# Optimization experiments

Hardware: AMD Instinct MI355X
Metric: run time of the kernel (lower is better)

## Reference

```python
import jax, jax.numpy as jnp
import numpy as np

B, D, L, C, N = 4096, 256, 4, 2048, 100000
MARGIN = 0.2
EPS = 1e-12  # F.normalize eps


def _l2norm(x):
    return x / jnp.clip(jnp.linalg.norm(x, axis=-1, keepdims=True), EPS)


def setup_inputs() -> dict:
    key = jax.random.key(0)
    k1, k2, k3, k4 = jax.random.split(key, 4)
    anchors = jax.random.normal(k1, (B, D), dtype=jnp.float32)
    centroids = jax.random.normal(k2, (L, C, D), dtype=jnp.float32)
    # unique cluster labels 0..C-1 within each eps level
    centroid_labels = jnp.tile(jnp.arange(C, dtype=jnp.int32), (L, 1))
    # DBSCAN labels in {-1, 0, ..., C-1}; -1 = noise (no positive at that eps)
    labels_per_eps = jax.random.randint(k3, (L, N), 0, C + 1, dtype=jnp.int32) - 1
    local_indices = jax.random.randint(k4, (B,), 0, N, dtype=jnp.int32)
    return {
        "anchors": anchors,
        "centroids": centroids,
        "centroid_labels": centroid_labels,
        "labels_per_eps": labels_per_eps,
        "local_indices": local_indices,
    }


def reference(anchors, centroids, centroid_labels, labels_per_eps, local_indices):
    an = _l2norm(anchors)                                   # [B, D]
    cent = _l2norm(jax.lax.stop_gradient(centroids))        # centroids detached in original
    flat_c = cent.reshape(L * C, D)                         # [M, D]
    flat_eps = jnp.repeat(jnp.arange(L, dtype=jnp.int32), C)  # [M] eps id of each centroid
    flat_lab = centroid_labels.reshape(-1)                  # [M]

    anchor_labels = labels_per_eps[:, local_indices].T      # [B, L]
    lab_at = anchor_labels[:, flat_eps]                     # [B, M] anchor's label at centroid's eps
    pos = (lab_at == flat_lab[None, :]) & (lab_at != -1)    # [B, M] positive-centroid mask

    sim = an @ flat_c.T                                     # [B, M] cosine sims
    sim_ap = jnp.min(jnp.where(pos, sim, 2.0), axis=1)      # hardest positive (min sim)
    sim_an = jnp.max(jnp.where(pos, -2.0, sim), axis=1)     # hardest negative (max sim)

    has_pos = jnp.any(pos, axis=1)
    has_neg = jnp.any(~pos, axis=1)
    valid = has_pos & has_neg

    per = jnp.maximum(sim_an - sim_ap + MARGIN, 0.0)        # [B]
    cnt = jnp.sum(valid.astype(jnp.float32))
    loss = jnp.sum(jnp.where(valid, per, 0.0)) / jnp.maximum(cnt, 1.0)
    return loss
```

## Files before the change

### kernel.cpp

```cpp
#include <hip/hip_runtime.h>
#include <hip/hip_bf16.h>

#define BB 4096
#define DD 256
#define LL 4
#define CC 2048
#define NN 100000

typedef unsigned int uint32;

using f32x16 = __attribute__((ext_vector_type(16))) float;
using bf16x8 = __attribute__((ext_vector_type(8))) __bf16;

#define GLD16(g, l)                                                        \
    __builtin_amdgcn_global_load_lds(                                      \
        (const __attribute__((address_space(1))) unsigned int*)(g),        \
        (__attribute__((address_space(3))) unsigned int*)(l), 16, 0, 0)

__device__ __forceinline__ uint32 f2ord(float f) {
    uint32 u = __float_as_uint(f);
    return (u & 0x80000000u) ? ~u : (u | 0x80000000u);
}
__device__ __forceinline__ float ord2f(uint32 u) {
    u = (u & 0x80000000u) ? (u & 0x7FFFFFFFu) : ~u;
    return __uint_as_float(u);
}
__device__ __forceinline__ unsigned short bf16bits(float f) {
    __hip_bfloat16 h = __float2bfloat16(f);
    unsigned short b;
    __builtin_memcpy(&b, &h, 2);
    return b;
}


__global__ __launch_bounds__(256) void prep_all(const float* __restrict__ anchors,
                                                const float* __restrict__ centroids,
                                                const int* __restrict__ lpe,
                                                const int* __restrict__ li,
                                                unsigned short* __restrict__ Ah,
                                                unsigned short* __restrict__ Al,
                                                unsigned short* __restrict__ Ch,
                                                unsigned short* __restrict__ Cl,
                                                int* __restrict__ pos_col) {
    const int bid = blockIdx.x;
    if (bid >= 3072) {
        int t = (bid - 3072) * 256 + threadIdx.x;
        int l = t >> 12, b = t & 4095;
        pos_col[l * BB + b] = lpe[l * NN + li[b]];
        return;
    }
    const bool is_a = (bid < 1024);
    const float* src = is_a ? anchors : centroids;
    unsigned short* hi = is_a ? Ah : Ch;
    unsigned short* lo = is_a ? Al : Cl;
    const int rb = is_a ? bid : (bid - 1024);
    int row = rb * 4 + (threadIdx.x >> 6);
    int lane = threadIdx.x & 63;
    float4 v = *reinterpret_cast<const float4*>(src + (size_t)row * DD + lane * 4);
    float ss = v.x * v.x + v.y * v.y + v.z * v.z + v.w * v.w;
    #pragma unroll
    for (int m = 1; m < 64; m <<= 1) ss += __shfl_xor(ss, m);
    float inv = 1.0f / fmaxf(sqrtf(ss), 1e-12f);
    float y0 = v.x * inv, y1 = v.y * inv, y2 = v.z * inv, y3 = v.w * inv;
    ushort4 h, l;
    h.x = bf16bits(y0); l.x = bf16bits(y0 - __bfloat162float(__float2bfloat16(y0)));
    h.y = bf16bits(y1); l.y = bf16bits(y1 - __bfloat162float(__float2bfloat16(y1)));
    h.z = bf16bits(y2); l.z = bf16bits(y2 - __bfloat162float(__float2bfloat16(y2)));
    h.w = bf16bits(y3); l.w = bf16bits(y3 - __bfloat162float(__float2bfloat16(y3)));
    *reinterpret_cast<ushort4*>(hi + (size_t)row * DD + lane * 4) = h;
    *reinterpret_cast<ushort4*>(lo + (size_t)row * DD + lane * 4) = l;
}

__global__ __launch_bounds__(256, 4) void mfma_main(
    const unsigned short* __restrict__ Ah, const unsigned short* __restrict__ Al,
    const unsigned short* __restrict__ Bh, const unsigned short* __restrict__ Bl,
    const int* __restrict__ clab, const int* __restrict__ pos_col,
    float* __restrict__ pn, float* __restrict__ pp) {
    __shared__ __align__(16) char smem[32768];

    const int tid = threadIdx.x;
    const int lane = tid & 63;
    const int w = tid >> 6;
    const int wr = w >> 1, wc = w & 1;

    const int bid = blockIdx.x;
    const int xcd = bid & 7, inner = bid >> 3;
    const int bx = (xcd & 1) * 16 + (inner & 15);
    const int by = (xcd >> 1) * 16 + (inner >> 4);
    const int mb = bx * 128, nb = by * 128;
    const int lev = nb >> 11;

    const unsigned short* arr = (w == 0) ? Ah : (w == 1) ? Al : (w == 2) ? Bh : Bl;
    const int pbase = (w < 2) ? mb : nb;
    const int sblk = (lane & 3) ^ ((lane >> 3) & 3);
    const unsigned short* gbase =
        arr + (size_t)(pbase + (lane >> 2)) * DD + sblk * 8;
    char* lbase = smem + w * 8192;

    f32x16 zero = {};
    f32x16 acc[2][2];
    #pragma unroll
    for (int i = 0; i < 2; ++i)
        #pragma unroll
        for (int j = 0; j < 2; ++j) acc[i][j] = zero;

    const int hw = lane >> 5;
    const int l31 = lane & 31;
    const int bswz = (lane >> 1) & 3;

    for (int t = 0; t < 8; ++t) {
        __syncthreads();
        #pragma unroll
        for (int s = 0; s < 8; ++s)
            GLD16(gbase + s * 16 * DD + t * 32, lbase + s * 1024);
        __syncthreads();

        #pragma unroll
        for (int tt = 0; tt < 2; ++tt) {
            const int phys = (((tt * 2 + hw) ^ bswz) << 4);
            bf16x8 fah[2], fal[2], fbh[2], fbl[2];
            #pragma unroll
            for (int i = 0; i < 2; ++i) {
                const int ra = (wr * 64 + i * 32 + l31) * 64 + phys;
                fah[i] = *reinterpret_cast<const bf16x8*>(smem + ra);
                fal[i] = *reinterpret_cast<const bf16x8*>(smem + 8192 + ra);
                const int rb2 = (wc * 64 + i * 32 + l31) * 64 + phys;
                fbh[i] = *reinterpret_cast<const bf16x8*>(smem + 16384 + rb2);
                fbl[i] = *reinterpret_cast<const bf16x8*>(smem + 24576 + rb2);
            }
            #pragma unroll
            for (int i = 0; i < 2; ++i)
                #pragma unroll
                for (int j = 0; j < 2; ++j) {
                    acc[i][j] = __builtin_amdgcn_mfma_f32_32x32x16_bf16(
                        fah[i], fbh[j], acc[i][j], 0, 0, 0);
                    acc[i][j] = __builtin_amdgcn_mfma_f32_32x32x16_bf16(
                        fah[i], fbl[j], acc[i][j], 0, 0, 0);
                    acc[i][j] = __builtin_amdgcn_mfma_f32_32x32x16_bf16(
                        fal[i], fbh[j], acc[i][j], 0, 0, 0);
                }
        }
    }

    __syncthreads();
    float* Ln = reinterpret_cast<float*>(smem);
    float* Lp = reinterpret_cast<float*>(smem + 1024);

    const int cl0 = clab[nb + wc * 64 + l31];
    const int cl1 = clab[nb + wc * 64 + 32 + l31];
    #pragma unroll
    for (int i = 0; i < 2; ++i) {
        const int rl0 = wr * 64 + i * 32;
        #pragma unroll
        for (int q = 0; q < 4; ++q) {
            const int4 pc4 = *reinterpret_cast<const int4*>(
                &pos_col[lev * BB + mb + rl0 + 8 * q + 4 * hw]);
            #pragma unroll
            for (int e = 0; e < 4; ++e) {
                const int reg = 4 * q + e;
                const int pcv = (e == 0) ? pc4.x : (e == 1) ? pc4.y : (e == 2) ? pc4.z : pc4.w;
                const float s0 = acc[i][0][reg];
                const float s1 = acc[i][1][reg];
                const bool p0 = (pcv == cl0) && (pcv >= 0);
                const bool p1 = (pcv == cl1) && (pcv >= 0);
                float nm = fmaxf(p0 ? -2.f : s0, p1 ? -2.f : s1);
                float pm = fminf(p0 ? s0 : 2.f, p1 ? s1 : 2.f);
                #pragma unroll
                for (int m = 1; m < 32; m <<= 1) {
                    nm = fmaxf(nm, __shfl_xor(nm, m));
                    pm = fminf(pm, __shfl_xor(pm, m));
                }
                if (l31 == 0) {
                    const int idx = wc * 128 + rl0 + 8 * q + e + hw * 4;
                    Ln[idx] = nm;
                    Lp[idx] = pm;
                }
            }
        }
    }
    __syncthreads();
    if (tid < 128) {
        const float nm = fmaxf(Ln[tid], Ln[128 + tid]);
        const float pm = fminf(Lp[tid], Lp[128 + tid]);
        pn[(size_t)by * BB + mb + tid] = nm;
        pp[(size_t)by * BB + mb + tid] = pm;
    }
}

__global__ __launch_bounds__(256) void finalize1(const float* __restrict__ pn,
                                                 const float* __restrict__ pp,
                                                 float* __restrict__ partials) {
    const int tid = threadIdx.x;
    const int row = blockIdx.x * 256 + tid;
    float nm = -2.f, pm = 2.f;
    for (int y = 0; y < 64; ++y) {
        nm = fmaxf(nm, pn[(size_t)y * BB + row]);
        pm = fminf(pm, pp[(size_t)y * BB + row]);
    }
    float sum = 0.f, cnt = 0.f;
    if (pm < 1.5f) {
        sum = fmaxf(nm - pm + 0.2f, 0.f);
        cnt = 1.f;
    }
    #pragma unroll
    for (int m = 1; m < 64; m <<= 1) {
        sum += __shfl_xor(sum, m);
        cnt += __shfl_xor(cnt, m);
    }
    __shared__ float s4[4], c4[4];
    if ((tid & 63) == 0) { s4[tid >> 6] = sum; c4[tid >> 6] = cnt; }
    __syncthreads();
    if (tid == 0) {
        partials[blockIdx.x] = s4[0] + s4[1] + s4[2] + s4[3];
        partials[16 + blockIdx.x] = c4[0] + c4[1] + c4[2] + c4[3];
    }
}

__global__ void finalize2(const float* __restrict__ partials, float* __restrict__ out) {
    if (threadIdx.x == 0) {
        float S = 0.f, C = 0.f;
        for (int i = 0; i < 16; ++i) { S += partials[i]; C += partials[16 + i]; }
        out[0] = S / fmaxf(C, 1.f);
    }
}


__global__ __launch_bounds__(256) void inv_norms(const float* __restrict__ src,
                                                 float* __restrict__ dst, int nrows) {
    int row = blockIdx.x * 4 + (threadIdx.x >> 6);
    int lane = threadIdx.x & 63;
    if (row >= nrows) return;
    float4 v = *reinterpret_cast<const float4*>(src + (size_t)row * DD + lane * 4);
    float ss = v.x * v.x + v.y * v.y + v.z * v.z + v.w * v.w;
    #pragma unroll
    for (int m = 1; m < 64; m <<= 1) ss += __shfl_xor(ss, m);
    if (lane == 0) dst[row] = 1.0f / fmaxf(sqrtf(ss), 1e-12f);
}

__global__ __launch_bounds__(256) void prep_fb(const int* __restrict__ labels_per_eps,
                                               const int* __restrict__ local_indices,
                                               int* __restrict__ pos_col,
                                               uint32* __restrict__ ap_key,
                                               uint32* __restrict__ an_key) {
    int t = blockIdx.x * 256 + threadIdx.x;
    int b = t >> 2, l = t & 3;
    pos_col[t] = labels_per_eps[l * NN + local_indices[b]];
    if (t < BB) { ap_key[t] = f2ord(2.0f); an_key[t] = f2ord(-2.0f); }
}

__global__ __launch_bounds__(256, 4) void fp32_main(const float* __restrict__ A,
                                                    const float* __restrict__ Cm,
                                                    const float* __restrict__ inv_a,
                                                    const float* __restrict__ inv_c,
                                                    const int* __restrict__ clab,
                                                    const int* __restrict__ pos_col,
                                                    uint32* __restrict__ ap_key,
                                                    uint32* __restrict__ an_key) {
    __shared__ float4 As[64 * 17];
    __shared__ float4 Bs[16 * 64];
    const int tid = threadIdx.x;
    const int lane = tid & 63;
    const int wv = tid >> 6;
    const int mb = blockIdx.x * 64;
    const int colbase = blockIdx.y * 64;
    const int lev = colbase >> 11;
    const int kgS = tid & 15;
    const int rS = tid >> 4;
    float acc[16];
    #pragma unroll
    for (int r = 0; r < 16; ++r) acc[r] = 0.f;
    for (int kc = 0; kc < DD; kc += 64) {
        __syncthreads();
        #pragma unroll
        for (int i = 0; i < 4; ++i) {
            int r = rS + 16 * i;
            As[r * 17 + kgS] = *reinterpret_cast<const float4*>(
                A + (size_t)(mb + r) * DD + kc + kgS * 4);
            Bs[kgS * 64 + (r ^ (kgS & 7))] = *reinterpret_cast<const float4*>(
                Cm + (size_t)(colbase + r) * DD + kc + kgS * 4);
        }
        __syncthreads();
        #pragma unroll
        for (int kg = 0; kg < 16; ++kg) {
            float4 b = Bs[kg * 64 + (lane ^ (kg & 7))];
            #pragma unroll
            for (int r = 0; r < 16; ++r) {
                float4 a = As[(wv * 16 + r) * 17 + kg];
                acc[r] = fmaf(a.x, b.x, acc[r]);
                acc[r] = fmaf(a.y, b.y, acc[r]);
                acc[r] = fmaf(a.z, b.z, acc[r]);
                acc[r] = fmaf(a.w, b.w, acc[r]);
            }
        }
    }
    const float ic = inv_c[colbase + lane];
    const int cl = clab[colbase + lane];
    const int row0 = mb + wv * 16;
    #pragma unroll
    for (int r = 0; r < 16; ++r) {
        float s = acc[r] * inv_a[row0 + r] * ic;
        int pcr = pos_col[(row0 + r) * LL + lev];
        bool pos = (pcr == cl) && (pcr >= 0);
        float nm = pos ? -2.f : s;
        #pragma unroll
        for (int m = 1; m < 64; m <<= 1) nm = fmaxf(nm, __shfl_xor(nm, m));
        if (lane == 0) atomicMax(&an_key[row0 + r], f2ord(nm));
        if (pos) atomicMin(&ap_key[row0 + r], f2ord(s));
    }
}

__global__ __launch_bounds__(256) void fb_finalize(const uint32* __restrict__ ap_key,
                                                   const uint32* __restrict__ an_key,
                                                   float* __restrict__ out) {
    int tid = threadIdx.x;
    float sum = 0.f, cnt = 0.f;
    for (int b = tid; b < BB; b += 256) {
        float ap = ord2f(ap_key[b]);
        float an = ord2f(an_key[b]);
        if (ap < 1.5f) { sum += fmaxf(an - ap + 0.2f, 0.f); cnt += 1.f; }
    }
    #pragma unroll
    for (int m = 1; m < 64; m <<= 1) { sum += __shfl_xor(sum, m); cnt += __shfl_xor(cnt, m); }
    __shared__ float s4[4], c4[4];
    int w = tid >> 6;
    if ((tid & 63) == 0) { s4[w] = sum; c4[w] = cnt; }
    __syncthreads();
    if (tid == 0) {
        out[0] = (s4[0] + s4[1] + s4[2] + s4[3]) / fmaxf(c4[0] + c4[1] + c4[2] + c4[3], 1.f);
    }
}


extern "C" void kernel_launch(void* const* d_in, const int* in_sizes, int n_in,
                              void* d_out, int out_size, void* d_ws, size_t ws_size,
                              hipStream_t stream) {
    const float* anchors         = (const float*)d_in[0];
    const float* centroids       = (const float*)d_in[1];
    const int*   centroid_labels = (const int*)d_in[2];
    const int*   labels_per_eps  = (const int*)d_in[3];
    const int*   local_indices   = (const int*)d_in[4];
    float* out = (float*)d_out;

    const size_t MB = 1024 * 1024;
    if (ws_size >= 15 * MB) {
        char* ws = (char*)d_ws;
        unsigned short* Ah = (unsigned short*)(ws);
        unsigned short* Al = (unsigned short*)(ws + 2 * MB);
        unsigned short* Ch = (unsigned short*)(ws + 4 * MB);
        unsigned short* Cl = (unsigned short*)(ws + 8 * MB);
        int*   pos_col = (int*)(ws + 12 * MB);
        float* pn = (float*)(ws + 12 * MB + 256 * 1024);
        float* pp = (float*)(ws + 13 * MB + 256 * 1024);
        float* partials = (float*)(ws + 14 * MB + 256 * 1024);

        prep_all<<<3136, 256, 0, stream>>>(anchors, centroids, labels_per_eps,
                                           local_indices, Ah, Al, Ch, Cl, pos_col);
        mfma_main<<<2048, 256, 0, stream>>>(Ah, Al, Ch, Cl, centroid_labels,
                                            pos_col, pn, pp);
        finalize1<<<16, 256, 0, stream>>>(pn, pp, partials);
        finalize2<<<1, 64, 0, stream>>>(partials, out);
    } else {
        float*  inv_a  = (float*)d_ws;
        float*  inv_c  = inv_a + BB;
        int*    pos_col = (int*)(inv_c + LL * CC);
        uint32* ap_key = (uint32*)(pos_col + BB * LL);
        uint32* an_key = ap_key + BB;

        inv_norms<<<BB / 4, 256, 0, stream>>>(anchors, inv_a, BB);
        inv_norms<<<(LL * CC) / 4, 256, 0, stream>>>(centroids, inv_c, LL * CC);
        prep_fb<<<(BB * LL) / 256, 256, 0, stream>>>(labels_per_eps, local_indices,
                                                     pos_col, ap_key, an_key);
        fp32_main<<<dim3(BB / 64, 128), 256, 0, stream>>>(anchors, centroids, inv_a, inv_c,
                                                          centroid_labels, pos_col,
                                                          ap_key, an_key);
        fb_finalize<<<1, 256, 0, stream>>>(ap_key, an_key, out);
    }
}
```

Baseline: 148.6 us.

## Use single bf16 GEMM with per-group maxima and fp32 fixup of near-max candidates

Replaces the three-pass split-bf16 GEMM with a single bf16 pass that records the per-32-column-group hardest-negative maximum. A new fixup kernel recomputes in fp32 only those groups whose bf16 max lies within a 0.02 margin of the global max, and computes the single positive centroid similarity directly in fp32. The main loop also gains LDS double buffering so the next K slice loads while the current one feeds the MFMAs. The aim is to cut MFMA work roughly threefold and drop the lo-part buffers. The risk is that the fixed 0.02 margin must cover bf16 error, and the fixup assumes exactly one positive per level because labels are unique.

```diff
diff --git a/kernel.cpp b/kernel.cpp
--- a/kernel.cpp
+++ b/kernel.cpp
@@ -38,9 +38,9 @@
                                                 const int* __restrict__ lpe,
                                                 const int* __restrict__ li,
                                                 unsigned short* __restrict__ Ah,
-                                                unsigned short* __restrict__ Al,
                                                 unsigned short* __restrict__ Ch,
-                                                unsigned short* __restrict__ Cl,
+                                                float* __restrict__ inv_a,
+                                                float* __restrict__ inv_c,
                                                 int* __restrict__ pos_col) {
     const int bid = blockIdx.x;
     if (bid >= 3072) {
@@ -52,7 +52,6 @@
     const bool is_a = (bid < 1024);
     const float* src = is_a ? anchors : centroids;
     unsigned short* hi = is_a ? Ah : Ch;
-    unsigned short* lo = is_a ? Al : Cl;
     const int rb = is_a ? bid : (bid - 1024);
     int row = rb * 4 + (threadIdx.x >> 6);
     int lane = threadIdx.x & 63;
@@ -61,21 +60,19 @@
     #pragma unroll
     for (int m = 1; m < 64; m <<= 1) ss += __shfl_xor(ss, m);
     float inv = 1.0f / fmaxf(sqrtf(ss), 1e-12f);
-    float y0 = v.x * inv, y1 = v.y * inv, y2 = v.z * inv, y3 = v.w * inv;
-    ushort4 h, l;
-    h.x = bf16bits(y0); l.x = bf16bits(y0 - __bfloat162float(__float2bfloat16(y0)));
-    h.y = bf16bits(y1); l.y = bf16bits(y1 - __bfloat162float(__float2bfloat16(y1)));
-    h.z = bf16bits(y2); l.z = bf16bits(y2 - __bfloat162float(__float2bfloat16(y2)));
-    h.w = bf16bits(y3); l.w = bf16bits(y3 - __bfloat162float(__float2bfloat16(y3)));
+    ushort4 h;
+    h.x = bf16bits(v.x * inv);
+    h.y = bf16bits(v.y * inv);
+    h.z = bf16bits(v.z * inv);
+    h.w = bf16bits(v.w * inv);
     *reinterpret_cast<ushort4*>(hi + (size_t)row * DD + lane * 4) = h;
-    *reinterpret_cast<ushort4*>(lo + (size_t)row * DD + lane * 4) = l;
+    if (lane == 0) (is_a ? inv_a : inv_c)[row] = inv;
 }
 
 __global__ __launch_bounds__(256, 4) void mfma_main(
-    const unsigned short* __restrict__ Ah, const unsigned short* __restrict__ Al,
-    const unsigned short* __restrict__ Bh, const unsigned short* __restrict__ Bl,
+    const unsigned short* __restrict__ Ah, const unsigned short* __restrict__ Bh,
     const int* __restrict__ clab, const int* __restrict__ pos_col,
-    float* __restrict__ pn, float* __restrict__ pp) {
+    float* __restrict__ png) {
     __shared__ __align__(16) char smem[32768];
 
     const int tid = threadIdx.x;
@@ -90,12 +87,11 @@
     const int mb = bx * 128, nb = by * 128;
     const int lev = nb >> 11;
 
-    const unsigned short* arr = (w == 0) ? Ah : (w == 1) ? Al : (w == 2) ? Bh : Bl;
-    const int pbase = (w < 2) ? mb : nb;
+    const unsigned short* arr = (w < 2) ? Ah : Bh;
+    const int pbase = ((w < 2) ? mb : nb) + (w & 1) * 64;
     const int sblk = (lane & 3) ^ ((lane >> 3) & 3);
     const unsigned short* gbase =
         arr + (size_t)(pbase + (lane >> 2)) * DD + sblk * 8;
-    char* lbase = smem + w * 8192;
 
     f32x16 zero = {};
     f32x16 acc[2][2];
@@ -106,46 +102,45 @@
 
     const int hw = lane >> 5;
     const int l31 = lane & 31;
-    const int bswz = (lane >> 1) & 3;
-
+    const int bswz = (l31 >> 1) & 3;
+
+    #pragma unroll
+    for (int s = 0; s < 4; ++s)
+        GLD16(gbase + s * 16 * DD, smem + w * 4096 + s * 1024);
+    __syncthreads();
+
+    int buf = 0;
     for (int t = 0; t < 8; ++t) {
-        __syncthreads();
-        #pragma unroll
-        for (int s = 0; s < 8; ++s)
-            GLD16(gbase + s * 16 * DD + t * 32, lbase + s * 1024);
-        __syncthreads();
-
+        if (t < 7) {
+            char* lb = smem + (buf ^ 1) * 16384 + w * 4096;
+            #pragma unroll
+            for (int s = 0; s < 4; ++s)
+                GLD16(gbase + s * 16 * DD + (t + 1) * 32, lb + s * 1024);
+        }
+        const char* base = smem + buf * 16384;
         #pragma unroll
         for (int tt = 0; tt < 2; ++tt) {
             const int phys = (((tt * 2 + hw) ^ bswz) << 4);
-            bf16x8 fah[2], fal[2], fbh[2], fbl[2];
+            bf16x8 fa[2], fb[2];
             #pragma unroll
             for (int i = 0; i < 2; ++i) {
-                const int ra = (wr * 64 + i * 32 + l31) * 64 + phys;
-                fah[i] = *reinterpret_cast<const bf16x8*>(smem + ra);
-                fal[i] = *reinterpret_cast<const bf16x8*>(smem + 8192 + ra);
-                const int rb2 = (wc * 64 + i * 32 + l31) * 64 + phys;
-                fbh[i] = *reinterpret_cast<const bf16x8*>(smem + 16384 + rb2);
-                fbl[i] = *reinterpret_cast<const bf16x8*>(smem + 24576 + rb2);
+                fa[i] = *reinterpret_cast<const bf16x8*>(
+                    base + (wr * 64 + i * 32 + l31) * 64 + phys);
+                fb[i] = *reinterpret_cast<const bf16x8*>(
+                    base + 8192 + (wc * 64 + i * 32 + l31) * 64 + phys);
             }
             #pragma unroll
             for (int i = 0; i < 2; ++i)
                 #pragma unroll
-                for (int j = 0; j < 2; ++j) {
+                for (int j = 0; j < 2; ++j)
                     acc[i][j] = __builtin_amdgcn_mfma_f32_32x32x16_bf16(
-                        fah[i], fbh[j], acc[i][j], 0, 0, 0);
-                    acc[i][j] = __builtin_amdgcn_mfma_f32_32x32x16_bf16(
-                        fah[i], fbl[j], acc[i][j], 0, 0, 0);
-                    acc[i][j] = __builtin_amdgcn_mfma_f32_32x32x16_bf16(
-                        fal[i], fbh[j], acc[i][j], 0, 0, 0);
-                }
-        }
-    }
-
-    __syncthreads();
-    float* Ln = reinterpret_cast<float*>(smem);
-    float* Lp = reinterpret_cast<float*>(smem + 1024);
-
+                        fa[i], fb[j], acc[i][j], 0, 0, 0);
+        }
+        __syncthreads();
+        buf ^= 1;
+    }
+
+    float* Lg = reinterpret_cast<float*>(smem);
     const int cl0 = clab[nb + wc * 64 + l31];
     const int cl1 = clab[nb + wc * 64 + 32 + l31];
     #pragma unroll
@@ -158,69 +153,129 @@
             #pragma unroll
             for (int e = 0; e < 4; ++e) {
                 const int reg = 4 * q + e;
-                const int pcv = (e == 0) ? pc4.x : (e == 1) ? pc4.y : (e == 2) ? pc4.z : pc4.w;
-                const float s0 = acc[i][0][reg];
-                const float s1 = acc[i][1][reg];
-                const bool p0 = (pcv == cl0) && (pcv >= 0);
-                const bool p1 = (pcv == cl1) && (pcv >= 0);
-                float nm = fmaxf(p0 ? -2.f : s0, p1 ? -2.f : s1);
-                float pm = fminf(p0 ? s0 : 2.f, p1 ? s1 : 2.f);
+                const int pcv = (e == 0) ? pc4.x : (e == 1) ? pc4.y
+                              : (e == 2) ? pc4.z : pc4.w;
+                float n0 = ((pcv == cl0) && (pcv >= 0)) ? -2.f : acc[i][0][reg];
+                float n1 = ((pcv == cl1) && (pcv >= 0)) ? -2.f : acc[i][1][reg];
                 #pragma unroll
                 for (int m = 1; m < 32; m <<= 1) {
-                    nm = fmaxf(nm, __shfl_xor(nm, m));
-                    pm = fminf(pm, __shfl_xor(pm, m));
+                    n0 = fmaxf(n0, __shfl_xor(n0, m));
+                    n1 = fmaxf(n1, __shfl_xor(n1, m));
                 }
                 if (l31 == 0) {
-                    const int idx = wc * 128 + rl0 + 8 * q + e + hw * 4;
-                    Ln[idx] = nm;
-                    Lp[idx] = pm;
+                    const int rloc = rl0 + 8 * q + e + 4 * hw;
+                    Lg[(wc * 2 + 0) * 128 + rloc] = n0;
+                    Lg[(wc * 2 + 1) * 128 + rloc] = n1;
                 }
             }
         }
     }
     __syncthreads();
-    if (tid < 128) {
-        const float nm = fmaxf(Ln[tid], Ln[128 + tid]);
-        const float pm = fminf(Lp[tid], Lp[128 + tid]);
-        pn[(size_t)by * BB + mb + tid] = nm;
-        pp[(size_t)by * BB + mb + tid] = pm;
-    }
-}
-
-__global__ __launch_bounds__(256) void finalize1(const float* __restrict__ pn,
-                                                 const float* __restrict__ pp,
-                                                 float* __restrict__ partials) {
-    const int tid = threadIdx.x;
-    const int row = blockIdx.x * 256 + tid;
-    float nm = -2.f, pm = 2.f;
-    for (int y = 0; y < 64; ++y) {
-        nm = fmaxf(nm, pn[(size_t)y * BB + row]);
-        pm = fminf(pm, pp[(size_t)y * BB + row]);
-    }
+    #pragma unroll
+    for (int s = 0; s < 2; ++s) {
+        const int idx = s * 256 + tid;
+        const int gl = idx >> 7, r = idx & 127;
+        png[(size_t)(by * 4 + gl) * BB + mb + r] = Lg[idx];
+    }
+}
+
+__global__ __launch_bounds__(256) void fixup(const float* __restrict__ anchors,
+                                             const float* __restrict__ centroids,
+                                             const float* __restrict__ inv_a,
+                                             const float* __restrict__ inv_c,
+                                             const int* __restrict__ clab,
+                                             const int* __restrict__ pos_col,
+                                             const float* __restrict__ png,
+                                             float* __restrict__ per,
+                                             float* __restrict__ vld) {
+    const int b = blockIdx.x;
+    const int tid = threadIdx.x, lane = tid & 63, w = tid >> 6;
+    __shared__ float af[256];
+    __shared__ float shn[4], shp[4], shg[4];
+
+    af[tid] = anchors[(size_t)b * DD + tid] * inv_a[b];
+    __syncthreads();
+
+    const float gv = png[(size_t)tid * BB + b];
+    float gm = gv;
+    #pragma unroll
+    for (int m = 1; m < 64; m <<= 1) gm = fmaxf(gm, __shfl_xor(gm, m));
+    if (lane == 0) shg[w] = gm;
+    __syncthreads();
+    const float gmax = fmaxf(fmaxf(shg[0], shg[1]), fmaxf(shg[2], shg[3]));
+
+    const int pcv = pos_col[w * BB + b];
+    float best = -2.f;
+    unsigned long long mball = __ballot(gv >= gmax - 0.02f);
+    while (mball) {
+        const int bit = __ffsll((long long)mball) - 1;
+        mball &= mball - 1;
+        const int g = w * 64 + bit;
+        const int col = g * 32 + (lane >> 1);
+        const float* cr = centroids + (size_t)col * DD + (lane & 1) * 128;
+        const float* ar = af + (lane & 1) * 128;
+        float s = 0.f;
+        #pragma unroll
+        for (int k2 = 0; k2 < 32; ++k2) {
+            float4 c4 = *reinterpret_cast<const float4*>(cr + k2 * 4);
+            float4 a4 = *reinterpret_cast<const float4*>(ar + k2 * 4);
+            s = fmaf(a4.x, c4.x, s); s = fmaf(a4.y, c4.y, s);
+            s = fmaf(a4.z, c4.z, s); s = fmaf(a4.w, c4.w, s);
+        }
+        s += __shfl_xor(s, 1);
+        float val = -2.f;
+        if ((lane & 1) == 0) {
+            const int cl = clab[col];
+            const bool pos = (pcv == cl) && (pcv >= 0);
+            val = pos ? -2.f : s * inv_c[col];
+        }
+        #pragma unroll
+        for (int m = 1; m < 64; m <<= 1) val = fmaxf(val, __shfl_xor(val, m));
+        best = fmaxf(best, val);
+    }
+    if (lane == 0) shn[w] = best;
+
+    float pv = 2.f;
+    if (pcv >= 0) {
+        const int col = w * CC + pcv;
+        float4 a4 = *reinterpret_cast<const float4*>(&af[lane * 4]);
+        float4 c4 = *reinterpret_cast<const float4*>(
+            centroids + (size_t)col * DD + lane * 4);
+        float s = a4.x * c4.x + a4.y * c4.y + a4.z * c4.z + a4.w * c4.w;
+        #pragma unroll
+        for (int m = 1; m < 64; m <<= 1) s += __shfl_xor(s, m);
+        if (clab[col] == pcv) pv = s * inv_c[col];
+    }
+    if (lane == 0) shp[w] = pv;
+    __syncthreads();
+    if (tid == 0) {
+        const float ng = fmaxf(fmaxf(shn[0], shn[1]), fmaxf(shn[2], shn[3]));
+        const float pm = fminf(fminf(shp[0], shp[1]), fminf(shp[2], shp[3]));
+        const bool valid = (pm < 1.5f);
+        per[b] = valid ? fmaxf(ng - pm + 0.2f, 0.f) : 0.f;
+        vld[b] = valid ? 1.f : 0.f;
+    }
+}
+
+__global__ __launch_bounds__(256) void final_reduce(const float* __restrict__ per,
+                                                    const float* __restrict__ vld,
+                                                    float* __restrict__ out) {
+    int tid = threadIdx.x;
     float sum = 0.f, cnt = 0.f;
-    if (pm < 1.5f) {
-        sum = fmaxf(nm - pm + 0.2f, 0.f);
-        cnt = 1.f;
-    }
+    for (int b = tid; b < BB; b += 256) { sum += per[b]; cnt += vld[b]; }
     #pragma unroll
     for (int m = 1; m < 64; m <<= 1) {
         sum += __shfl_xor(sum, m);
         cnt += __shfl_xor(cnt, m);
     }
     __shared__ float s4[4], c4[4];
-    if ((tid & 63) == 0) { s4[tid >> 6] = sum; c4[tid >> 6] = cnt; }
+    int w = tid >> 6;
+    if ((tid & 63) == 0) { s4[w] = sum; c4[w] = cnt; }
     __syncthreads();
     if (tid == 0) {
-        partials[blockIdx.x] = s4[0] + s4[1] + s4[2] + s4[3];
-        partials[16 + blockIdx.x] = c4[0] + c4[1] + c4[2] + c4[3];
-    }
-}
-
-__global__ void finalize2(const float* __restrict__ partials, float* __restrict__ out) {
-    if (threadIdx.x == 0) {
-        float S = 0.f, C = 0.f;
-        for (int i = 0; i < 16; ++i) { S += partials[i]; C += partials[16 + i]; }
-        out[0] = S / fmaxf(C, 1.f);
+        float S = s4[0] + s4[1] + s4[2] + s4[3];
+        float Cv = c4[0] + c4[1] + c4[2] + c4[3];
+        out[0] = S / fmaxf(Cv, 1.f);
     }
 }
 
@@ -345,20 +400,21 @@
     if (ws_size >= 15 * MB) {
         char* ws = (char*)d_ws;
         unsigned short* Ah = (unsigned short*)(ws);
-        unsigned short* Al = (unsigned short*)(ws + 2 * MB);
-        unsigned short* Ch = (unsigned short*)(ws + 4 * MB);
-        unsigned short* Cl = (unsigned short*)(ws + 8 * MB);
-        int*   pos_col = (int*)(ws + 12 * MB);
-        float* pn = (float*)(ws + 12 * MB + 256 * 1024);
-        float* pp = (float*)(ws + 13 * MB + 256 * 1024);
-        float* partials = (float*)(ws + 14 * MB + 256 * 1024);
+        unsigned short* Ch = (unsigned short*)(ws + 2 * MB);
+        float* inv_a  = (float*)(ws + 6 * MB);
+        float* inv_c  = (float*)(ws + 6 * MB + 16 * 1024);
+        int*   pos_col = (int*)(ws + 6 * MB + 48 * 1024);
+        float* png = (float*)(ws + 7 * MB);
+        float* per = (float*)(ws + 11 * MB);
+        float* vld = (float*)(ws + 11 * MB + 16 * 1024);
 
         prep_all<<<3136, 256, 0, stream>>>(anchors, centroids, labels_per_eps,
-                                           local_indices, Ah, Al, Ch, Cl, pos_col);
-        mfma_main<<<2048, 256, 0, stream>>>(Ah, Al, Ch, Cl, centroid_labels,
-                                            pos_col, pn, pp);
-        finalize1<<<16, 256, 0, stream>>>(pn, pp, partials);
-        finalize2<<<1, 64, 0, stream>>>(partials, out);
+                                           local_indices, Ah, Ch, inv_a, inv_c,
+                                           pos_col);
+        mfma_main<<<2048, 256, 0, stream>>>(Ah, Ch, centroid_labels, pos_col, png);
+        fixup<<<BB, 256, 0, stream>>>(anchors, centroids, inv_a, inv_c,
+                                      centroid_labels, pos_col, png, per, vld);
+        final_reduce<<<1, 256, 0, stream>>>(per, vld, out);
     } else {
         float*  inv_a  = (float*)d_ws;
         float*  inv_c  = inv_a + BB;
```

After: 218.8 us. +47.2%, slower.
